# Kernel tuning notes

Measured on AMD Instinct MI355X. Metric: run time of the kernel, lower is better.

The kernel has to match this reference:

```python
import jax, jax.numpy as jnp
import numpy as np

N, E, D, H, O = 100000, 1600000, 128, 128, 64


def setup_inputs() -> dict:
    key = jax.random.key(0)
    ks = jax.random.split(key, 9)
    x = jax.random.normal(ks[0], (N, D), dtype=jnp.float32)
    edge_index = jax.random.randint(ks[1], (2, E), 0, N, dtype=jnp.int64)
    edge_weight = jax.random.normal(ks[2], (E,), dtype=jnp.float32)
    s1 = 1.0 / np.sqrt(D)
    s2 = 1.0 / np.sqrt(H)
    W_rel1 = jax.random.normal(ks[3], (D, H), dtype=jnp.float32) * s1
    b_rel1 = jnp.zeros((H,), dtype=jnp.float32)
    W_root1 = jax.random.normal(ks[4], (D, H), dtype=jnp.float32) * s1
    W_rel2 = jax.random.normal(ks[5], (H, O), dtype=jnp.float32) * s2
    b_rel2 = jnp.zeros((O,), dtype=jnp.float32)
    W_root2 = jax.random.normal(ks[6], (H, O), dtype=jnp.float32) * s2
    return {"x": x, "edge_weight": edge_weight, "edge_index": edge_index,
            "W_rel1": W_rel1, "b_rel1": b_rel1, "W_root1": W_root1,
            "W_rel2": W_rel2, "b_rel2": b_rel2, "W_root2": W_root2}


def _graph_conv(h, src, dst, ew, W_rel, b_rel, W_root):
    # message: gather source features, scale by edge weight  [E, d]
    msg = h[src] * ew[:, None]
    # aggregate: sum messages into destination nodes  [N, d]
    aggr = jax.ops.segment_sum(msg, dst, num_segments=N)
    # GraphConv: lin_rel(aggr) + lin_root(h)
    return aggr @ W_rel + b_rel + h @ W_root


def reference(x, edge_weight, edge_index, W_rel1, b_rel1, W_root1, W_rel2, b_rel2, W_root2):
    src, dst = edge_index[0], edge_index[1]
    ew = jax.nn.sigmoid(edge_weight)  # edge_weighted=True path, applied once
    h = jax.nn.relu(_graph_conv(x, src, dst, ew, W_rel1, b_rel1, W_root1))
    out = _graph_conv(h, src, dst, ew, W_rel2, b_rel2, W_root2)
    return out
```

## Files before the change

### kernel.cpp

```cpp
#include <hip/hip_runtime.h>

#define NN 100000
#define EE 1600000
#define DD 128
#define HH 128
#define OO 64

#define NPART 8
#define MAXDEG 512
#define CAP 48
#define MAX_OVF 4096

typedef unsigned short u16;
typedef __attribute__((ext_vector_type(8))) short bf16x8;
typedef __attribute__((ext_vector_type(4))) float f32x4;

__device__ __forceinline__ u16 f2b(float f) {
  union { float f; unsigned u; } v; v.f = f;
  unsigned r = v.u + 0x7fffu + ((v.u >> 16) & 1u);
  return (u16)(r >> 16);
}
__device__ __forceinline__ float b2f(unsigned h) {
  union { unsigned u; float f; } v; v.u = h << 16;
  return v.f;
}
__device__ __forceinline__ void fma8(float* acc, uint4 v, float w) {
  acc[0] = fmaf(b2f(v.x & 0xffffu), w, acc[0]);
  acc[1] = fmaf(b2f(v.x >> 16), w, acc[1]);
  acc[2] = fmaf(b2f(v.y & 0xffffu), w, acc[2]);
  acc[3] = fmaf(b2f(v.y >> 16), w, acc[3]);
  acc[4] = fmaf(b2f(v.z & 0xffffu), w, acc[4]);
  acc[5] = fmaf(b2f(v.z >> 16), w, acc[5]);
  acc[6] = fmaf(b2f(v.w & 0xffffu), w, acc[6]);
  acc[7] = fmaf(b2f(v.w >> 16), w, acc[7]);
}

__global__ __launch_bounds__(256) void cvt_x_k(const float* __restrict__ x,
                                               u16* __restrict__ xb) {
  int i = blockIdx.x * 256 + threadIdx.x;
  if (i >= NN * DD / 8) return;
  const float4* p = reinterpret_cast<const float4*>(x) + (size_t)i * 2;
  float4 a = p[0], b = p[1];
  uint4 o;
  o.x = (unsigned)f2b(a.x) | ((unsigned)f2b(a.y) << 16);
  o.y = (unsigned)f2b(a.z) | ((unsigned)f2b(a.w) << 16);
  o.z = (unsigned)f2b(b.x) | ((unsigned)f2b(b.y) << 16);
  o.w = (unsigned)f2b(b.z) | ((unsigned)f2b(b.w) << 16);
  reinterpret_cast<uint4*>(xb)[i] = o;
}

__global__ __launch_bounds__(256) void cvt_w_k(
    const float* __restrict__ Wr1, const float* __restrict__ Wo1,
    const float* __restrict__ Wr2, const float* __restrict__ Wo2,
    u16* __restrict__ Wt1, u16* __restrict__ Wt2) {
  int i = blockIdx.x * 256 + threadIdx.x;
  if (i < 128 * 256) {
    int n = i >> 8, k = i & 255;
    float v = (k < 128) ? Wr1[k * 128 + n] : Wo1[(k - 128) * 128 + n];
    Wt1[i] = f2b(v);
  } else if (i < 128 * 256 + 64 * 256) {
    int j = i - 128 * 256;
    int n = j >> 8, k = j & 255;
    float v = (k < 128) ? Wr2[k * 64 + n] : Wo2[(k - 128) * 64 + n];
    Wt2[j] = f2b(v);
  }
}

__global__ __launch_bounds__(256) void fill_direct_k(
    const int* __restrict__ ei, const float* __restrict__ w,
    int* __restrict__ cnt, uint2* __restrict__ slots,
    uint4* __restrict__ ovf, int* __restrict__ ovf_cnt,
    int lo, int hi, int E) {
  int e = blockIdx.x * 256 + threadIdx.x;
  if (e >= E) return;
  int dst = ei[E + e];
  if (dst < lo || dst >= hi) return;
  int pos = atomicAdd(&cnt[dst], 1);
  float sig = 1.0f / (1.0f + expf(-w[e]));
  unsigned src = (unsigned)ei[e];
  if (pos < CAP) {
    slots[(size_t)dst * CAP + pos] = make_uint2(src, __float_as_uint(sig));
  } else {
    int o = atomicAdd(ovf_cnt, 1);
    if (o < MAX_OVF) ovf[o] = make_uint4((unsigned)dst, src, __float_as_uint(sig), 0u);
  }
}

__global__ __launch_bounds__(256) void dhist_k(const int* __restrict__ cnt,
                                               int* __restrict__ dhist) {
  __shared__ int lh[MAXDEG];
  for (int i = threadIdx.x; i < MAXDEG; i += 256) lh[i] = 0;
  __syncthreads();
  int n = blockIdx.x * 256 + threadIdx.x;
  if (n < NN) {
    int d = min(cnt[n], MAXDEG - 1);
    atomicAdd(&lh[d], 1);
  }
  __syncthreads();
  for (int i = threadIdx.x; i < MAXDEG; i += 256) {
    int c = lh[i];
    if (c) atomicAdd(&dhist[i], c);
  }
}

__global__ __launch_bounds__(MAXDEG) void dscan_k(int* __restrict__ dhist) {
  __shared__ int s[MAXDEG];
  const int t = threadIdx.x;
  int v = dhist[t];
  s[t] = v;
  __syncthreads();
#pragma unroll
  for (int off = 1; off < MAXDEG; off <<= 1) {
    int u = (t >= off) ? s[t - off] : 0;
    __syncthreads();
    s[t] += u;
    __syncthreads();
  }
  dhist[t] = s[t] - v;
}

__global__ __launch_bounds__(256) void dperm_k(const int* __restrict__ cnt,
                                               int* __restrict__ dcur,
                                               int* __restrict__ perm) {
  __shared__ int lh[MAXDEG];
  __shared__ int lbase[MAXDEG];
  for (int i = threadIdx.x; i < MAXDEG; i += 256) lh[i] = 0;
  __syncthreads();
  int n = blockIdx.x * 256 + threadIdx.x;
  int d = 0, lpos = 0;
  if (n < NN) {
    d = min(cnt[n], MAXDEG - 1);
    lpos = atomicAdd(&lh[d], 1);
  }
  __syncthreads();
  for (int i = threadIdx.x; i < MAXDEG; i += 256) {
    int c = lh[i];
    if (c) lbase[i] = atomicAdd(&dcur[i], c);
  }
  __syncthreads();
  if (n < NN) perm[lbase[d] + lpos] = n;
}

__global__ __launch_bounds__(256) void gather_k(
    const u16* __restrict__ feat, const int* __restrict__ cnt,
    const uint2* __restrict__ slots, const int* __restrict__ perm,
    u16* __restrict__ aggr) {
  int gid = blockIdx.x * 256 + threadIdx.x;
  int g = gid >> 4;
  int c = gid & 15;
  if (g >= NN) return;
  int node = perm[g];
  int count = min(cnt[node], CAP);
  const uint2* recs = slots + (size_t)node * CAP;
  float acc[8] = {0.f, 0.f, 0.f, 0.f, 0.f, 0.f, 0.f, 0.f};
  int e = 0;
  for (; e + 4 <= count; e += 4) {
    uint2 r0 = recs[e + 0];
    uint2 r1 = recs[e + 1];
    uint2 r2 = recs[e + 2];
    uint2 r3 = recs[e + 3];
    uint4 v0 = *reinterpret_cast<const uint4*>(feat + (size_t)r0.x * DD + c * 8);
    uint4 v1 = *reinterpret_cast<const uint4*>(feat + (size_t)r1.x * DD + c * 8);
    uint4 v2 = *reinterpret_cast<const uint4*>(feat + (size_t)r2.x * DD + c * 8);
    uint4 v3 = *reinterpret_cast<const uint4*>(feat + (size_t)r3.x * DD + c * 8);
    fma8(acc, v0, __uint_as_float(r0.y));
    fma8(acc, v1, __uint_as_float(r1.y));
    fma8(acc, v2, __uint_as_float(r2.y));
    fma8(acc, v3, __uint_as_float(r3.y));
  }
  for (; e < count; ++e) {
    uint2 r = recs[e];
    uint4 v = *reinterpret_cast<const uint4*>(feat + (size_t)r.x * DD + c * 8);
    fma8(acc, v, __uint_as_float(r.y));
  }
  uint4 o;
  o.x = (unsigned)f2b(acc[0]) | ((unsigned)f2b(acc[1]) << 16);
  o.y = (unsigned)f2b(acc[2]) | ((unsigned)f2b(acc[3]) << 16);
  o.z = (unsigned)f2b(acc[4]) | ((unsigned)f2b(acc[5]) << 16);
  o.w = (unsigned)f2b(acc[6]) | ((unsigned)f2b(acc[7]) << 16);
  *reinterpret_cast<uint4*>(aggr + (size_t)node * DD + c * 8) = o;
}

__global__ __launch_bounds__(256) void ovf_fix_k(const int* __restrict__ ovf_cnt,
                                                 const uint4* __restrict__ ovf,
                                                 const u16* __restrict__ feat,
                                                 u16* __restrict__ aggr) {
  int novf = min(*ovf_cnt, MAX_OVF);
  int gid = blockIdx.x * 256 + threadIdx.x;
  int idx = gid >> 6;
  int word = gid & 63;
  if (idx >= novf) return;
  uint4 r = ovf[idx];
  float wgt = __uint_as_float(r.z);
  unsigned fv = *reinterpret_cast<const unsigned*>(feat + (size_t)r.y * DD + word * 2);
  float m0 = b2f(fv & 0xffffu) * wgt;
  float m1 = b2f(fv >> 16) * wgt;
  unsigned* addr = reinterpret_cast<unsigned*>(aggr + (size_t)r.x * DD + word * 2);
  unsigned old = *addr, assumed;
  do {
    assumed = old;
    float a0 = b2f(assumed & 0xffffu) + m0;
    float a1 = b2f(assumed >> 16) + m1;
    unsigned nv = (unsigned)f2b(a0) | ((unsigned)f2b(a1) << 16);
    old = atomicCAS(addr, assumed, nv);
  } while (old != assumed);
}

template <int HO, bool RELU, bool OUTBF16>
__global__ __launch_bounds__(256) void gemm_mfma_k(
    const u16* __restrict__ A1, const u16* __restrict__ A2,
    const u16* __restrict__ Bt, const float* __restrict__ bias,
    void* __restrict__ Cout, int n_rows) {
  constexpr int CG = HO / 16;
  __shared__ u16 As[64][40];
  __shared__ u16 Bs[HO][40];

  const int t = threadIdx.x;
  const int w = t >> 6;
  const int lane = t & 63;
  const int row0 = blockIdx.x * 64;

  f32x4 acc[CG];
#pragma unroll
  for (int cg = 0; cg < CG; ++cg) acc[cg] = (f32x4){0.f, 0.f, 0.f, 0.f};

  const int arow = w * 16 + (lane & 15);
  const int kq = (lane >> 4) * 8;

  for (int k0 = 0; k0 < 256; k0 += 32) {
    {
      int node = t >> 2;
      int koff = (t & 3) * 8;
      int k = k0 + koff;
      int gr = row0 + node;
      uint4 v = make_uint4(0u, 0u, 0u, 0u);
      if (gr < n_rows) {
        const u16* src = (k < 128) ? (A1 + (size_t)gr * 128 + k)
                                   : (A2 + (size_t)gr * 128 + (k - 128));
        v = *reinterpret_cast<const uint4*>(src);
      }
      *reinterpret_cast<uint4*>(&As[node][koff]) = v;
    }
#pragma unroll
    for (int i = 0; i < CG / 4; ++i) {
      int c2 = t + i * 256;
      int n = c2 >> 2;
      int koff = (c2 & 3) * 8;
      uint4 v = *reinterpret_cast<const uint4*>(Bt + (size_t)n * 256 + k0 + koff);
      *reinterpret_cast<uint4*>(&Bs[n][koff]) = v;
    }
    __syncthreads();

    bf16x8 a = *reinterpret_cast<const bf16x8*>(&As[arow][kq]);
#pragma unroll
    for (int cg = 0; cg < CG; ++cg) {
      bf16x8 b = *reinterpret_cast<const bf16x8*>(&Bs[cg * 16 + (lane & 15)][kq]);
      acc[cg] = __builtin_amdgcn_mfma_f32_16x16x32_bf16(a, b, acc[cg], 0, 0, 0);
    }
    __syncthreads();
  }

  const int rbase = w * 16 + ((lane >> 4) << 2);
#pragma unroll
  for (int cg = 0; cg < CG; ++cg) {
    int col = cg * 16 + (lane & 15);
    float bia = bias[col];
#pragma unroll
    for (int j = 0; j < 4; ++j) {
      int gr = row0 + rbase + j;
      if (gr < n_rows) {
        float v = acc[cg][j] + bia;
        if (RELU) v = fmaxf(v, 0.f);
        if (OUTBF16) ((u16*)Cout)[(size_t)gr * HO + col] = f2b(v);
        else ((float*)Cout)[(size_t)gr * HO + col] = v;
      }
    }
  }
}

extern "C" void kernel_launch(void* const* d_in, const int* in_sizes, int n_in,
                              void* d_out, int out_size, void* d_ws, size_t ws_size,
                              hipStream_t stream) {
  const float* x   = (const float*)d_in[0];
  const float* w   = (const float*)d_in[1];
  const int*   ei  = (const int*)d_in[2];
  const float* Wr1 = (const float*)d_in[3];
  const float* br1 = (const float*)d_in[4];
  const float* Wo1 = (const float*)d_in[5];
  const float* Wr2 = (const float*)d_in[6];
  const float* br2 = (const float*)d_in[7];
  const float* Wo2 = (const float*)d_in[8];
  float* out = (float*)d_out;

  char* ws = (char*)d_ws;
  int*   cnt     = (int*)(ws);
  int*   ovf_cnt = (int*)(ws + 400000);
  int*   dhist   = (int*)(ws + 401024);
  int*   perm    = (int*)(ws + 403072);
  uint4* ovf     = (uint4*)(ws + 803072);
  uint2* slots   = (uint2*)(ws + 868608);
  u16*   xb      = (u16*)(ws + 39268608);
  u16*   hb      = (u16*)(ws + 64868608);
  u16*   aggrb   = (u16*)(ws + 90468608);
  u16*   Wt1     = (u16*)(ws + 116068608);
  u16*   Wt2     = (u16*)(ws + 116134144);

  const int egrid = (EE + 255) / 256;
  const int ngrid = (NN + 255) / 256;

  cvt_x_k<<<NN * DD / 8 / 256, 256, 0, stream>>>(x, xb);
  cvt_w_k<<<(192 * 256 + 255) / 256, 256, 0, stream>>>(Wr1, Wo1, Wr2, Wo2, Wt1, Wt2);

  hipMemsetAsync(cnt, 0, 403072, stream);
  {
    const int pstep = (NN + NPART - 1) / NPART;
    for (int p = 0; p < NPART; ++p) {
      int lo = p * pstep;
      int hi = min(NN, lo + pstep);
      fill_direct_k<<<egrid, 256, 0, stream>>>(ei, w, cnt, slots, ovf, ovf_cnt, lo, hi, EE);
    }
  }

  dhist_k<<<ngrid, 256, 0, stream>>>(cnt, dhist);
  dscan_k<<<1, MAXDEG, 0, stream>>>(dhist);
  dperm_k<<<ngrid, 256, 0, stream>>>(cnt, dhist, perm);

  const int ggrid = (NN * 16 + 255) / 256;
  const int mgrid = (NN + 63) / 64;
  const int ogrid = (MAX_OVF * 64) / 256;

  gather_k<<<ggrid, 256, 0, stream>>>(xb, cnt, slots, perm, aggrb);
  ovf_fix_k<<<ogrid, 256, 0, stream>>>(ovf_cnt, ovf, xb, aggrb);
  gemm_mfma_k<HH, true, true><<<mgrid, 256, 0, stream>>>(aggrb, xb, Wt1, br1, hb, NN);

  gather_k<<<ggrid, 256, 0, stream>>>(hb, cnt, slots, perm, aggrb);
  ovf_fix_k<<<ogrid, 256, 0, stream>>>(ovf_cnt, ovf, hb, aggrb);
  gemm_mfma_k<OO, false, false><<<mgrid, 256, 0, stream>>>(aggrb, hb, Wt2, br2, out, NN);
}
```

Baseline: 310.6 us.

## Pad per-node counters, shrink slot capacity, and deepen gather unroll

Per-node edge counters are padded to a 64-byte stride so atomics on different destinations land in different cache lines. Slot capacity per node drops from 48 to 32, which enlarges the overflow buffer, and the edge fill uses 4 partition passes instead of 8. The gather loop now issues 8 independent feature loads per iteration for more memory-level parallelism. The costs are a 6.4MB counter array that must be zeroed and read with a stride, more edges going through the overflow path, and more register use in the gather.

```diff
diff --git a/kernel.cpp b/kernel.cpp
--- a/kernel.cpp
+++ b/kernel.cpp
@@ -6,10 +6,11 @@
 #define HH 128
 #define OO 64
 
-#define NPART 8
+#define NPART 4
 #define MAXDEG 512
-#define CAP 48
-#define MAX_OVF 4096
+#define CAP 32
+#define MAX_OVF 16384
+#define CSTRIDE 16
 
 typedef unsigned short u16;
 typedef __attribute__((ext_vector_type(8))) short bf16x8;
@@ -68,14 +69,14 @@
 
 __global__ __launch_bounds__(256) void fill_direct_k(
     const int* __restrict__ ei, const float* __restrict__ w,
-    int* __restrict__ cnt, uint2* __restrict__ slots,
+    int* __restrict__ cntp, uint2* __restrict__ slots,
     uint4* __restrict__ ovf, int* __restrict__ ovf_cnt,
     int lo, int hi, int E) {
   int e = blockIdx.x * 256 + threadIdx.x;
   if (e >= E) return;
   int dst = ei[E + e];
   if (dst < lo || dst >= hi) return;
-  int pos = atomicAdd(&cnt[dst], 1);
+  int pos = atomicAdd(&cntp[dst * CSTRIDE], 1);
   float sig = 1.0f / (1.0f + expf(-w[e]));
   unsigned src = (unsigned)ei[e];
   if (pos < CAP) {
@@ -86,14 +87,14 @@
   }
 }
 
-__global__ __launch_bounds__(256) void dhist_k(const int* __restrict__ cnt,
+__global__ __launch_bounds__(256) void dhist_k(const int* __restrict__ cntp,
                                                int* __restrict__ dhist) {
   __shared__ int lh[MAXDEG];
   for (int i = threadIdx.x; i < MAXDEG; i += 256) lh[i] = 0;
   __syncthreads();
   int n = blockIdx.x * 256 + threadIdx.x;
   if (n < NN) {
-    int d = min(cnt[n], MAXDEG - 1);
+    int d = min(cntp[n * CSTRIDE], MAXDEG - 1);
     atomicAdd(&lh[d], 1);
   }
   __syncthreads();
@@ -119,7 +120,7 @@
   dhist[t] = s[t] - v;
 }
 
-__global__ __launch_bounds__(256) void dperm_k(const int* __restrict__ cnt,
+__global__ __launch_bounds__(256) void dperm_k(const int* __restrict__ cntp,
                                                int* __restrict__ dcur,
                                                int* __restrict__ perm) {
   __shared__ int lh[MAXDEG];
@@ -129,7 +130,7 @@
   int n = blockIdx.x * 256 + threadIdx.x;
   int d = 0, lpos = 0;
   if (n < NN) {
-    d = min(cnt[n], MAXDEG - 1);
+    d = min(cntp[n * CSTRIDE], MAXDEG - 1);
     lpos = atomicAdd(&lh[d], 1);
   }
   __syncthreads();
@@ -142,7 +143,7 @@
 }
 
 __global__ __launch_bounds__(256) void gather_k(
-    const u16* __restrict__ feat, const int* __restrict__ cnt,
+    const u16* __restrict__ feat, const int* __restrict__ cntp,
     const uint2* __restrict__ slots, const int* __restrict__ perm,
     u16* __restrict__ aggr) {
   int gid = blockIdx.x * 256 + threadIdx.x;
@@ -150,23 +151,32 @@
   int c = gid & 15;
   if (g >= NN) return;
   int node = perm[g];
-  int count = min(cnt[node], CAP);
+  int count = min(cntp[node * CSTRIDE], CAP);
   const uint2* recs = slots + (size_t)node * CAP;
   float acc[8] = {0.f, 0.f, 0.f, 0.f, 0.f, 0.f, 0.f, 0.f};
   int e = 0;
-  for (; e + 4 <= count; e += 4) {
-    uint2 r0 = recs[e + 0];
-    uint2 r1 = recs[e + 1];
-    uint2 r2 = recs[e + 2];
-    uint2 r3 = recs[e + 3];
-    uint4 v0 = *reinterpret_cast<const uint4*>(feat + (size_t)r0.x * DD + c * 8);
-    uint4 v1 = *reinterpret_cast<const uint4*>(feat + (size_t)r1.x * DD + c * 8);
-    uint4 v2 = *reinterpret_cast<const uint4*>(feat + (size_t)r2.x * DD + c * 8);
-    uint4 v3 = *reinterpret_cast<const uint4*>(feat + (size_t)r3.x * DD + c * 8);
-    fma8(acc, v0, __uint_as_float(r0.y));
-    fma8(acc, v1, __uint_as_float(r1.y));
-    fma8(acc, v2, __uint_as_float(r2.y));
-    fma8(acc, v3, __uint_as_float(r3.y));
+  for (; e + 8 <= count; e += 8) {
+    uint2 r[8];
+#pragma unroll
+    for (int j = 0; j < 8; ++j) r[j] = recs[e + j];
+    uint4 v[8];
+#pragma unroll
+    for (int j = 0; j < 8; ++j)
+      v[j] = *reinterpret_cast<const uint4*>(feat + (size_t)r[j].x * DD + c * 8);
+#pragma unroll
+    for (int j = 0; j < 8; ++j) fma8(acc, v[j], __uint_as_float(r[j].y));
+  }
+  if (e + 4 <= count) {
+    uint2 r[4];
+#pragma unroll
+    for (int j = 0; j < 4; ++j) r[j] = recs[e + j];
+    uint4 v[4];
+#pragma unroll
+    for (int j = 0; j < 4; ++j)
+      v[j] = *reinterpret_cast<const uint4*>(feat + (size_t)r[j].x * DD + c * 8);
+#pragma unroll
+    for (int j = 0; j < 4; ++j) fma8(acc, v[j], __uint_as_float(r[j].y));
+    e += 4;
   }
   for (; e < count; ++e) {
     uint2 r = recs[e];
@@ -293,17 +303,17 @@
   float* out = (float*)d_out;
 
   char* ws = (char*)d_ws;
-  int*   cnt     = (int*)(ws);
-  int*   ovf_cnt = (int*)(ws + 400000);
-  int*   dhist   = (int*)(ws + 401024);
-  int*   perm    = (int*)(ws + 403072);
-  uint4* ovf     = (uint4*)(ws + 803072);
-  uint2* slots   = (uint2*)(ws + 868608);
-  u16*   xb      = (u16*)(ws + 39268608);
-  u16*   hb      = (u16*)(ws + 64868608);
-  u16*   aggrb   = (u16*)(ws + 90468608);
-  u16*   Wt1     = (u16*)(ws + 116068608);
-  u16*   Wt2     = (u16*)(ws + 116134144);
+  int*   cntp    = (int*)(ws);
+  int*   ovf_cnt = (int*)(ws + 6400000);
+  int*   dhist   = (int*)(ws + 6401024);
+  int*   perm    = (int*)(ws + 6403072);
+  uint4* ovf     = (uint4*)(ws + 6803072);
+  uint2* slots   = (uint2*)(ws + 7065216);
+  u16*   xb      = (u16*)(ws + 32665216);
+  u16*   hb      = (u16*)(ws + 58265216);
+  u16*   aggrb   = (u16*)(ws + 83865216);
+  u16*   Wt1     = (u16*)(ws + 109465216);
+  u16*   Wt2     = (u16*)(ws + 109530752);
 
   const int egrid = (EE + 255) / 256;
   const int ngrid = (NN + 255) / 256;
@@ -311,29 +321,29 @@
   cvt_x_k<<<NN * DD / 8 / 256, 256, 0, stream>>>(x, xb);
   cvt_w_k<<<(192 * 256 + 255) / 256, 256, 0, stream>>>(Wr1, Wo1, Wr2, Wo2, Wt1, Wt2);
 
-  hipMemsetAsync(cnt, 0, 403072, stream);
+  hipMemsetAsync(cntp, 0, 6403072, stream);
   {
     const int pstep = (NN + NPART - 1) / NPART;
     for (int p = 0; p < NPART; ++p) {
       int lo = p * pstep;
       int hi = min(NN, lo + pstep);
-      fill_direct_k<<<egrid, 256, 0, stream>>>(ei, w, cnt, slots, ovf, ovf_cnt, lo, hi, EE);
-    }
-  }
-
-  dhist_k<<<ngrid, 256, 0, stream>>>(cnt, dhist);
+      fill_direct_k<<<egrid, 256, 0, stream>>>(ei, w, cntp, slots, ovf, ovf_cnt, lo, hi, EE);
+    }
+  }
+
+  dhist_k<<<ngrid, 256, 0, stream>>>(cntp, dhist);
   dscan_k<<<1, MAXDEG, 0, stream>>>(dhist);
-  dperm_k<<<ngrid, 256, 0, stream>>>(cnt, dhist, perm);
+  dperm_k<<<ngrid, 256, 0, stream>>>(cntp, dhist, perm);
 
   const int ggrid = (NN * 16 + 255) / 256;
   const int mgrid = (NN + 63) / 64;
   const int ogrid = (MAX_OVF * 64) / 256;
 
-  gather_k<<<ggrid, 256, 0, stream>>>(xb, cnt, slots, perm, aggrb);
+  gather_k<<<ggrid, 256, 0, stream>>>(xb, cntp, slots, perm, aggrb);
   ovf_fix_k<<<ogrid, 256, 0, stream>>>(ovf_cnt, ovf, xb, aggrb);
   gemm_mfma_k<HH, true, true><<<mgrid, 256, 0, stream>>>(aggrb, xb, Wt1, br1, hb, NN);
 
-  gather_k<<<ggrid, 256, 0, stream>>>(hb, cnt, slots, perm, aggrb);
+  gather_k<<<ggrid, 256, 0, stream>>>(hb, cntp, slots, perm, aggrb);
   ovf_fix_k<<<ogrid, 256, 0, stream>>>(ovf_cnt, ovf, hb, aggrb);
   gemm_mfma_k<OO, false, false><<<mgrid, 256, 0, stream>>>(aggrb, hb, Wt2, br2, out, NN);
 }
```

New measurement: 296.0 us. 1.05x faster.
